# Optimization experiments

Hardware: AMD Instinct MI355X
Metric: run time of the kernel (lower is better)

The kernel has to match this reference:

```python
import jax, jax.numpy as jnp
import numpy as np

N_NODES = 50000
N_EDGES = 1600000


def gcn_conv(x, edge_index, W, b):
    """PyG GCNConv: linear transform, add self-loops, symmetric deg^-1/2 norm, scatter-add."""
    n = x.shape[0]
    h = x @ W  # [N, out]
    loop = jnp.arange(n)
    src = jnp.concatenate([edge_index[0], loop])
    dst = jnp.concatenate([edge_index[1], loop])
    ones = jnp.ones(src.shape[0], dtype=h.dtype)
    deg = jax.ops.segment_sum(ones, dst, num_segments=n)  # in-degree incl. self-loop
    dinv = jnp.where(deg > 0, jax.lax.rsqrt(deg), 0.0)
    norm = dinv[src] * dinv[dst]  # [E+N]
    msg = h[src] * norm[:, None]  # gathered, normalized messages
    out = jax.ops.segment_sum(msg, dst, num_segments=n)
    return out + b


def setup_inputs() -> dict:
    key = jax.random.key(0)
    k1, k2, k3, k4 = jax.random.split(key, 4)
    x = jax.random.normal(k1, (N_NODES, 512), dtype=jnp.float32)
    edge_index = jax.random.randint(k2, (2, N_EDGES), 0, N_NODES, dtype=jnp.int64)
    W1 = jax.random.normal(k3, (512, 128), dtype=jnp.float32) * (1.0 / np.sqrt(512))
    b1 = jnp.zeros((128,), dtype=jnp.float32)
    W2 = jax.random.normal(k4, (128, 40), dtype=jnp.float32) * (1.0 / np.sqrt(128))
    b2 = jnp.zeros((40,), dtype=jnp.float32)
    return {"x": x, "edge_index": edge_index, "W1": W1, "b1": b1, "W2": W2, "b2": b2}


def reference(x, edge_index, W1, b1, W2, b2):
    h = gcn_conv(x, edge_index, W1, b1)
    h = jax.nn.relu(h)
    h = gcn_conv(h, edge_index, W2, b2)
    return jax.nn.log_softmax(h, axis=1)
```

## Files before the change

### kernel.cpp

```cpp
#include <hip/hip_runtime.h>
#include <hip/hip_bf16.h>
#include <math.h>


#define FEAT1 512
#define FEAT2 128
#define FEAT3 40

typedef __attribute__((ext_vector_type(8))) short bf16x8;
typedef __attribute__((ext_vector_type(4))) float f32x4;

__device__ __forceinline__ unsigned short f2bf(float f) {
    union { float f; unsigned u; } c; c.f = f;
    unsigned r = c.u + 0x7fff + ((c.u >> 16) & 1);
    return (unsigned short)(r >> 16);
}
__device__ __forceinline__ float bf2f(unsigned v16) {
    union { unsigned u; float f; } c; c.u = v16 << 16;
    return c.f;
}

__device__ __forceinline__ bf16x8 pack_bf8(f32x4 a, f32x4 b) {
    union { __hip_bfloat162 h[4]; bf16x8 v; } u;
    u.h[0] = __float22bfloat162_rn(make_float2(a[0], a[1]));
    u.h[1] = __float22bfloat162_rn(make_float2(a[2], a[3]));
    u.h[2] = __float22bfloat162_rn(make_float2(b[0], b[1]));
    u.h[3] = __float22bfloat162_rn(make_float2(b[2], b[3]));
    return u.v;
}

__device__ __forceinline__ int load_src(const int* ei, long e, long E, int f64) {
    return f64 ? ei[2 * e] : ei[e];
}
__device__ __forceinline__ int load_dst(const int* ei, long e, long E, int f64) {
    return f64 ? ei[2 * E + 2 * e] : ei[E + e];
}

__launch_bounds__(1024)
__global__ void partA_kernel(const int* __restrict__ ei,
                             int* __restrict__ gbkt, unsigned* __restrict__ part,
                             int bktCap, long E, int NB) {
    __shared__ int hist[256], lbase[256], lcur[256];
    __shared__ int anyv;
    int t = threadIdx.x;
    if (t == 0) anyv = 0;
    if (t < 256) { hist[t] = 0; lcur[t] = 0; }
    __syncthreads();
    if (t < 256 && ei[2 * t + 1] != 0) anyv = 1;
    __syncthreads();
    int f64 = (anyv == 0) ? 1 : 0;

    long chunk = (E + gridDim.x - 1) / gridDim.x;
    long start = (long)blockIdx.x * chunk;
    long end = start + chunk; if (end > E) end = E;

    for (long e0 = start; e0 < end; e0 += 1024) {
        long e = e0 + t;
        if (e < end) {
            int dst = load_dst(ei, e, E, f64);
            atomicAdd(&hist[dst >> 8], 1);
        }
    }
    __syncthreads();
    if (t < NB && hist[t]) lbase[t] = atomicAdd(&gbkt[t], hist[t]);
    __syncthreads();

    for (long e0 = start; e0 < end; e0 += 1024) {
        long e = e0 + t;
        if (e < end) {
            int src = load_src(ei, e, E, f64);
            int dst = load_dst(ei, e, E, f64);
            int bkt = dst >> 8;
            int pos = lbase[bkt] + atomicAdd(&lcur[bkt], 1);
            if (pos < bktCap)
                part[(long)bkt * bktCap + pos] = (unsigned)src | ((unsigned)(dst & 255) << 17);
        }
    }
}

__launch_bounds__(256)
__global__ void partB_kernel(const unsigned* __restrict__ part, int bktCap,
                             const int* __restrict__ gbkt,
                             int* __restrict__ offsets, float* __restrict__ dinv,
                             int* __restrict__ col, int N, int E) {
    __shared__ int h[256], sc[256], cur[256];
    int b = blockIdx.x, t = threadIdx.x;
    int NB = gridDim.x;

    sc[t] = (t < NB) ? gbkt[t] : 0;
    __syncthreads();
    #pragma unroll
    for (int d = 1; d < 256; d <<= 1) {
        int tv = (t >= d) ? sc[t - d] : 0;
        __syncthreads();
        sc[t] += tv;
        __syncthreads();
    }
    int base = (b == 0) ? 0 : sc[b - 1];
    if (b == 0 && t == 0) offsets[N] = E;

    int n = gbkt[b]; if (n > bktCap) n = bktCap;
    int lo = b << 8;
    const unsigned* p = part + (long)b * bktCap;
    h[t] = 0;
    __syncthreads();
    for (int i = t; i < n; i += 256) atomicAdd(&h[(p[i] >> 17) & 255], 1);
    __syncthreads();
    int cnt = h[t];
    sc[t] = cnt;
    __syncthreads();
    #pragma unroll
    for (int d = 1; d < 256; d <<= 1) {
        int tv = (t >= d) ? sc[t - d] : 0;
        __syncthreads();
        sc[t] += tv;
        __syncthreads();
    }
    int ex = sc[t] - cnt;
    int node = lo + t;
    if (node < N) {
        offsets[node] = base + ex;
        dinv[node] = 1.0f / sqrtf((float)(cnt + 1));
    }
    cur[t] = ex;
    __syncthreads();
    for (int i = t; i < n; i += 256) {
        unsigned u = p[i];
        int r = atomicAdd(&cur[(u >> 17) & 255], 1);
        col[base + r] = u & 0x1FFFF;
    }
}

__global__ void wbt_kernel(const float* __restrict__ W1, const float* __restrict__ W2,
                           unsigned short* __restrict__ Bt, unsigned short* __restrict__ Bt2,
                           int* __restrict__ gbkt) {
    int b = blockIdx.x;
    if (b == 0 && threadIdx.x < 256) gbkt[threadIdx.x] = 0;
    if (b < FEAT2) {
        int r = b, x7 = r & 7;
        for (int k = threadIdx.x; k < FEAT1; k += blockDim.x) {
            int c = k >> 3, j = k & 7;
            int eo = (((c ^ x7) << 3) | j);
            Bt[(long)r * FEAT1 + eo] = f2bf(W1[(long)k * FEAT2 + r]);
        }
    } else {
        int n = b - FEAT2;
        for (int k = threadIdx.x; k < FEAT2; k += blockDim.x)
            Bt2[(long)n * FEAT2 + k] = (n < FEAT3) ? f2bf(W2[(long)k * FEAT3 + n]) : 0;
    }
}

#define G1_NW 8
__launch_bounds__(512, 2)
__global__ void gemm1_mfma_kernel(const float* __restrict__ A,
                                  const unsigned short* __restrict__ Bsw,
                                  const float* __restrict__ dinv,
                                  unsigned short* __restrict__ C, int M) {
    __shared__ unsigned short Bl[FEAT2 * FEAT1];
    int t = threadIdx.x;

    {
        uint4 tmp[16];
        #pragma unroll
        for (int r = 0; r < 16; r++)
            tmp[r] = *(const uint4*)((const char*)Bsw + (size_t)t * 16 + (size_t)r * 8192);
        #pragma unroll
        for (int r = 0; r < 16; r++)
            *(uint4*)((char*)Bl + (size_t)t * 16 + (size_t)r * 8192) = tmp[r];
    }
    __syncthreads();

    int w = t >> 6, lane = t & 63;
    int quad = lane >> 4, r15 = lane & 15;
    int row0 = (blockIdx.x * (G1_NW * 2) + w * 2) * 16;
    int x7 = r15 & 7;

    int ar0 = row0 + r15;      if (ar0 >= M) ar0 = M - 1;
    int ar1 = row0 + 16 + r15; if (ar1 >= M) ar1 = M - 1;
    const float* ap0 = A + (long)ar0 * FEAT1 + quad * 8;
    const float* ap1 = A + (long)ar1 * FEAT1 + quad * 8;

    f32x4 ra0[3][2], ra1[3][2];
    #pragma unroll
    for (int p = 0; p < 3; p++) {
        ra0[p][0] = *(const f32x4*)(ap0 + p * 32);
        ra0[p][1] = *(const f32x4*)(ap0 + p * 32 + 4);
        ra1[p][0] = *(const f32x4*)(ap1 + p * 32);
        ra1[p][1] = *(const f32x4*)(ap1 + p * 32 + 4);
    }

    f32x4 acc0[8], acc1[8];
    #pragma unroll
    for (int nt = 0; nt < 8; nt++) {
        acc0[nt] = (f32x4){0.f, 0.f, 0.f, 0.f};
        acc1[nt] = (f32x4){0.f, 0.f, 0.f, 0.f};
    }

    #pragma unroll
    for (int ks = 0; ks < 16; ks++) {
        int sl = ks % 3;
        bf16x8 af0 = pack_bf8(ra0[sl][0], ra0[sl][1]);
        bf16x8 af1 = pack_bf8(ra1[sl][0], ra1[sl][1]);
        if (ks < 13) {
            ra0[sl][0] = *(const f32x4*)(ap0 + (ks + 3) * 32);
            ra0[sl][1] = *(const f32x4*)(ap0 + (ks + 3) * 32 + 4);
            ra1[sl][0] = *(const f32x4*)(ap1 + (ks + 3) * 32);
            ra1[sl][1] = *(const f32x4*)(ap1 + (ks + 3) * 32 + 4);
        }
        #pragma unroll
        for (int nt = 0; nt < 8; nt++) {
            int eo = (nt * 16 + r15) * FEAT1 + (((ks * 4 + quad) ^ x7) << 3);
            bf16x8 bfrag = *(const bf16x8*)(Bl + eo);
            acc0[nt] = __builtin_amdgcn_mfma_f32_16x16x32_bf16(af0, bfrag, acc0[nt], 0, 0, 0);
            acc1[nt] = __builtin_amdgcn_mfma_f32_16x16x32_bf16(af1, bfrag, acc1[nt], 0, 0, 0);
        }
    }

    #pragma unroll
    for (int tile = 0; tile < 2; tile++) {
        #pragma unroll
        for (int reg = 0; reg < 4; reg++) {
            int orow = row0 + tile * 16 + quad * 4 + reg;
            if (orow < M) {
                float di = dinv[orow];
                #pragma unroll
                for (int nt = 0; nt < 8; nt++) {
                    float v = (tile == 0) ? acc0[nt][reg] : acc1[nt][reg];
                    C[(long)orow * FEAT2 + nt * 16 + r15] = f2bf(v * di);
                }
            }
        }
    }
}

__launch_bounds__(256)
__global__ void agg1_kernel(const unsigned short* __restrict__ h1s,
                            const int* __restrict__ col, const int* __restrict__ off,
                            const float* __restrict__ dinv, const float* __restrict__ b1,
                            unsigned short* __restrict__ a1, int N) {
    int node = blockIdx.x * 4 + (threadIdx.x >> 6);
    if (node >= N) return;
    int l = threadIdx.x & 63;
    int q = l >> 4, j = l & 15;
    const unsigned short* hp = h1s + 8 * j;
    int o0 = off[node], o1 = off[node + 1];
    float s0 = 0.f, s1 = 0.f, s2 = 0.f, s3 = 0.f,
          s4 = 0.f, s5 = 0.f, s6 = 0.f, s7 = 0.f;

    #define ACC8(P)                                                     \
        do {                                                            \
            s0 += __uint_as_float((P).x << 16);                         \
            s1 += __uint_as_float((P).x & 0xffff0000u);                 \
            s2 += __uint_as_float((P).y << 16);                         \
            s3 += __uint_as_float((P).y & 0xffff0000u);                 \
            s4 += __uint_as_float((P).z << 16);                         \
            s5 += __uint_as_float((P).z & 0xffff0000u);                 \
            s6 += __uint_as_float((P).w << 16);                         \
            s7 += __uint_as_float((P).w & 0xffff0000u);                 \
        } while (0)

    for (int base = o0; base < o1; base += 64) {
        int cnt = min(64, o1 - base);
        int myc = (l < cnt) ? col[base + l] : 0;
        int quads = cnt >> 2;
        int i = 0;
        for (; i + 2 <= quads; i += 2) {
            int c0 = __shfl(myc, 4 * i + q);
            int c1 = __shfl(myc, 4 * i + 4 + q);
            uint4 p0 = *(const uint4*)(hp + (long)c0 * FEAT2);
            uint4 p1 = *(const uint4*)(hp + (long)c1 * FEAT2);
            ACC8(p0);
            ACC8(p1);
        }
        if (i < quads) {
            int c0 = __shfl(myc, 4 * i + q);
            uint4 p0 = *(const uint4*)(hp + (long)c0 * FEAT2);
            ACC8(p0);
        }
        int e = (quads << 2) + q;
        int ec = e < 64 ? e : 0;
        int ct = __shfl(myc, ec);
        if (e < cnt) {
            uint4 p0 = *(const uint4*)(hp + (long)ct * FEAT2);
            ACC8(p0);
        }
    }
    #undef ACC8

    s0 += __shfl_xor(s0, 16); s1 += __shfl_xor(s1, 16);
    s2 += __shfl_xor(s2, 16); s3 += __shfl_xor(s3, 16);
    s4 += __shfl_xor(s4, 16); s5 += __shfl_xor(s5, 16);
    s6 += __shfl_xor(s6, 16); s7 += __shfl_xor(s7, 16);
    s0 += __shfl_xor(s0, 32); s1 += __shfl_xor(s1, 32);
    s2 += __shfl_xor(s2, 32); s3 += __shfl_xor(s3, 32);
    s4 += __shfl_xor(s4, 32); s5 += __shfl_xor(s5, 32);
    s6 += __shfl_xor(s6, 32); s7 += __shfl_xor(s7, 32);

    if (q == 0) {
        uint4 pv = *(const uint4*)(hp + (long)node * FEAT2);
        s0 += __uint_as_float(pv.x << 16); s1 += __uint_as_float(pv.x & 0xffff0000u);
        s2 += __uint_as_float(pv.y << 16); s3 += __uint_as_float(pv.y & 0xffff0000u);
        s4 += __uint_as_float(pv.z << 16); s5 += __uint_as_float(pv.z & 0xffff0000u);
        s6 += __uint_as_float(pv.w << 16); s7 += __uint_as_float(pv.w & 0xffff0000u);
        float di = dinv[node];
        float4 ba = *(const float4*)(b1 + 8 * j);
        float4 bb = *(const float4*)(b1 + 8 * j + 4);
        float v0 = s0 * di + ba.x, v1 = s1 * di + ba.y;
        float v2 = s2 * di + ba.z, v3 = s3 * di + ba.w;
        float v4 = s4 * di + bb.x, v5 = s5 * di + bb.y;
        float v6 = s6 * di + bb.z, v7 = s7 * di + bb.w;
        v0 = v0 > 0.f ? v0 : 0.f; v1 = v1 > 0.f ? v1 : 0.f;
        v2 = v2 > 0.f ? v2 : 0.f; v3 = v3 > 0.f ? v3 : 0.f;
        v4 = v4 > 0.f ? v4 : 0.f; v5 = v5 > 0.f ? v5 : 0.f;
        v6 = v6 > 0.f ? v6 : 0.f; v7 = v7 > 0.f ? v7 : 0.f;
        uint4 o;
        o.x = (unsigned)f2bf(v0) | ((unsigned)f2bf(v1) << 16);
        o.y = (unsigned)f2bf(v2) | ((unsigned)f2bf(v3) << 16);
        o.z = (unsigned)f2bf(v4) | ((unsigned)f2bf(v5) << 16);
        o.w = (unsigned)f2bf(v6) | ((unsigned)f2bf(v7) << 16);
        *(uint4*)(a1 + (long)node * FEAT2 + 8 * j) = o;
    }
}

__launch_bounds__(256)
__global__ void gemm2_mfma_kernel(const unsigned short* __restrict__ A,
                                  const unsigned short* __restrict__ Bt2,
                                  const float* __restrict__ dinv,
                                  unsigned short* __restrict__ C, int M) {
    int wave = blockIdx.x * (blockDim.x >> 6) + (threadIdx.x >> 6);
    int lane = threadIdx.x & 63;
    int quad = lane >> 4, r15 = lane & 15;
    int row0 = wave * 16;
    if (row0 >= M) return;
    int arow = row0 + r15;
    if (arow >= M) arow = M - 1;

    bf16x8 af[4];
    const unsigned short* ap = A + (long)arow * FEAT2 + quad * 8;
    #pragma unroll
    for (int ks = 0; ks < 4; ks++) af[ks] = *(const bf16x8*)(ap + ks * 32);

    f32x4 acc[3];
    #pragma unroll
    for (int nt = 0; nt < 3; nt++) acc[nt] = (f32x4){0.f, 0.f, 0.f, 0.f};
    #pragma unroll
    for (int ks = 0; ks < 4; ks++) {
        #pragma unroll
        for (int nt = 0; nt < 3; nt++) {
            bf16x8 bf = *(const bf16x8*)(Bt2 + (long)(nt * 16 + r15) * FEAT2 + ks * 32 + quad * 8);
            acc[nt] = __builtin_amdgcn_mfma_f32_16x16x32_bf16(af[ks], bf, acc[nt], 0, 0, 0);
        }
    }

    #pragma unroll
    for (int reg = 0; reg < 4; reg++) {
        int orow = row0 + quad * 4 + reg;
        if (orow >= M) continue;
        float di = dinv[orow];
        #pragma unroll
        for (int nt = 0; nt < 3; nt++) {
            int ocol = nt * 16 + r15;
            if (ocol < FEAT3)
                C[(long)orow * FEAT3 + ocol] = f2bf(acc[nt][reg] * di);
        }
    }
}

__launch_bounds__(256)
__global__ void agg2_lsm_kernel(const unsigned short* __restrict__ h2s,
                                const int* __restrict__ col, const int* __restrict__ off,
                                const float* __restrict__ dinv, const float* __restrict__ b2,
                                float* __restrict__ out, int N) {
    int node = blockIdx.x * 4 + (threadIdx.x >> 6);
    if (node >= N) return;
    int l = threadIdx.x & 63;
    bool act = l < FEAT3 / 2;
    int o0 = off[node], o1 = off[node + 1];
    float ax = 0.f, ay = 0.f;
    for (int base = o0; base < o1; base += 64) {
        int cnt = min(64, o1 - base);
        int myc = (l < cnt) ? col[base + l] : 0;
        int e = 0;
        for (; e + 4 <= cnt; e += 4) {
            int s0 = __shfl(myc, e + 0);
            int s1 = __shfl(myc, e + 1);
            int s2 = __shfl(myc, e + 2);
            int s3 = __shfl(myc, e + 3);
            if (act) {
                unsigned p0 = *(const unsigned*)(h2s + (long)s0 * FEAT3 + 2 * l);
                unsigned p1 = *(const unsigned*)(h2s + (long)s1 * FEAT3 + 2 * l);
                unsigned p2 = *(const unsigned*)(h2s + (long)s2 * FEAT3 + 2 * l);
                unsigned p3 = *(const unsigned*)(h2s + (long)s3 * FEAT3 + 2 * l);
                ax += bf2f(p0 & 0xffffu) + bf2f(p1 & 0xffffu) +
                      bf2f(p2 & 0xffffu) + bf2f(p3 & 0xffffu);
                ay += bf2f(p0 >> 16) + bf2f(p1 >> 16) + bf2f(p2 >> 16) + bf2f(p3 >> 16);
            }
        }
        for (; e < cnt; ++e) {
            int s = __shfl(myc, e);
            if (act) {
                unsigned p = *(const unsigned*)(h2s + (long)s * FEAT3 + 2 * l);
                ax += bf2f(p & 0xffffu);
                ay += bf2f(p >> 16);
            }
        }
    }
    float vx = -INFINITY, vy = -INFINITY;
    if (act) {
        unsigned pv = *(const unsigned*)(h2s + (long)node * FEAT3 + 2 * l);
        float di = dinv[node];
        float2 b = *(const float2*)(b2 + 2 * l);
        vx = (ax + bf2f(pv & 0xffffu)) * di + b.x;
        vy = (ay + bf2f(pv >> 16)) * di + b.y;
    }
    float m = fmaxf(vx, vy);
    #pragma unroll
    for (int o = 32; o >= 1; o >>= 1) m = fmaxf(m, __shfl_xor(m, o));
    float e = act ? (expf(vx - m) + expf(vy - m)) : 0.f;
    #pragma unroll
    for (int o = 32; o >= 1; o >>= 1) e += __shfl_xor(e, o);
    float ls = logf(e);
    if (act) {
        *(float2*)(out + (long)node * FEAT3 + 2 * l) = make_float2(vx - m - ls, vy - m - ls);
    }
}

extern "C" void kernel_launch(void* const* d_in, const int* in_sizes, int n_in,
                              void* d_out, int out_size, void* d_ws, size_t ws_size,
                              hipStream_t stream) {
    const float* x  = (const float*)d_in[0];
    const int*   ei = (const int*)d_in[1];
    const float* W1 = (const float*)d_in[2];
    const float* b1 = (const float*)d_in[3];
    const float* W2 = (const float*)d_in[4];
    const float* b2 = (const float*)d_in[5];
    float* out = (float*)d_out;

    const int  N = in_sizes[0] / FEAT1;
    const long E = in_sizes[1] / 2;

    char* ws = (char*)d_ws;
    size_t off = 0;
    auto alloc = [&](size_t bytes) -> void* {
        off = (off + 255) & ~(size_t)255;
        void* p = ws + off;
        off += bytes;
        return p;
    };
    const int NB = (N + 255) >> 8;
    const int bktCap = (int)(E / NB) + 1024;
    int*   offsets = (int*)alloc((size_t)(N + 1) * 4);
    float* dinv    = (float*)alloc((size_t)N * 4);
    int*   col     = (int*)alloc((size_t)E * 4);
    unsigned short* h1s = (unsigned short*)alloc((size_t)N * FEAT2 * 2);
    unsigned short* a1  = (unsigned short*)alloc((size_t)N * FEAT2 * 2);
    unsigned short* h2s = (unsigned short*)alloc((size_t)N * FEAT3 * 2);
    unsigned short* Bt  = (unsigned short*)alloc((size_t)FEAT2 * FEAT1 * 2);
    unsigned short* Bt2 = (unsigned short*)alloc((size_t)48 * FEAT2 * 2);
    unsigned* part = (unsigned*)alloc((size_t)NB * bktCap * 4);
    int*   gbkt    = (int*)alloc(256 * 4);
    int*   flagp   = (int*)alloc(4);
    (void)flagp;

    wbt_kernel<<<176, 256, 0, stream>>>(W1, W2, Bt, Bt2, gbkt);
    partA_kernel<<<256, 1024, 0, stream>>>(ei, gbkt, part, bktCap, E, NB);
    partB_kernel<<<NB, 256, 0, stream>>>(part, bktCap, gbkt, offsets, dinv, col, N, (int)E);
    {
        int tiles  = (N + 15) / 16;
        int blocks = (tiles + G1_NW * 2 - 1) / (G1_NW * 2);
        gemm1_mfma_kernel<<<blocks, 512, 0, stream>>>(x, Bt, dinv, h1s, N);
    }
    agg1_kernel<<<(N + 3) / 4, 256, 0, stream>>>(h1s, col, offsets, dinv, b1, a1, N);
    gemm2_mfma_kernel<<<(N / 16 + 3) / 4, 256, 0, stream>>>(a1, Bt2, dinv, h2s, N);
    agg2_lsm_kernel<<<(N + 3) / 4, 256, 0, stream>>>(h2s, col, offsets, dinv, b2, out, N);
}
```

Baseline: 318.7 us.

## Split agg1 into two feature-half passes, widen agg2 gathers, register-cache edges in partition

The layer-1 aggregation now runs as two launches, each covering 64 of the 128 features, so eight edges are gathered concurrently per wavefront and each pass touches a smaller slice of h1s. The layer-2 aggregation with log-softmax now uses 16-lane groups, each loading four bf16 features per edge, so four edges are processed in parallel and the partial sums are reduced with shuffles. The partition kernel keeps each thread's seven edges in registers between the histogram pass and the scatter pass instead of reading the edge list twice. The tradeoffs are a second pass over the CSR column data and two extra reduction stages, and EPT=7 only covers every edge when each block's chunk is at most 7×1024 edges, which holds for the grid size used here.

```diff
diff --git a/kernel.cpp b/kernel.cpp
--- a/kernel.cpp
+++ b/kernel.cpp
@@ -29,13 +29,7 @@
     return u.v;
 }
 
-__device__ __forceinline__ int load_src(const int* ei, long e, long E, int f64) {
-    return f64 ? ei[2 * e] : ei[e];
-}
-__device__ __forceinline__ int load_dst(const int* ei, long e, long E, int f64) {
-    return f64 ? ei[2 * E + 2 * e] : ei[E + e];
-}
-
+#define EPT 7
 __launch_bounds__(1024)
 __global__ void partA_kernel(const int* __restrict__ ei,
                              int* __restrict__ gbkt, unsigned* __restrict__ part,
@@ -49,31 +43,40 @@
     if (t < 256 && ei[2 * t + 1] != 0) anyv = 1;
     __syncthreads();
     int f64 = (anyv == 0) ? 1 : 0;
+    const long long* ei64 = (const long long*)ei;
 
     long chunk = (E + gridDim.x - 1) / gridDim.x;
     long start = (long)blockIdx.x * chunk;
     long end = start + chunk; if (end > E) end = E;
 
-    for (long e0 = start; e0 < end; e0 += 1024) {
-        long e = e0 + t;
+    int srcs[EPT], dsts[EPT];
+    #pragma unroll
+    for (int r = 0; r < EPT; r++) {
+        long e = start + (long)r * 1024 + t;
         if (e < end) {
-            int dst = load_dst(ei, e, E, f64);
-            atomicAdd(&hist[dst >> 8], 1);
+            if (f64) {
+                srcs[r] = (int)ei64[e];
+                dsts[r] = (int)ei64[E + e];
+            } else {
+                srcs[r] = ei[e];
+                dsts[r] = ei[E + e];
+            }
+            atomicAdd(&hist[dsts[r] >> 8], 1);
         }
     }
     __syncthreads();
     if (t < NB && hist[t]) lbase[t] = atomicAdd(&gbkt[t], hist[t]);
     __syncthreads();
 
-    for (long e0 = start; e0 < end; e0 += 1024) {
-        long e = e0 + t;
+    #pragma unroll
+    for (int r = 0; r < EPT; r++) {
+        long e = start + (long)r * 1024 + t;
         if (e < end) {
-            int src = load_src(ei, e, E, f64);
-            int dst = load_dst(ei, e, E, f64);
-            int bkt = dst >> 8;
+            int bkt = dsts[r] >> 8;
             int pos = lbase[bkt] + atomicAdd(&lcur[bkt], 1);
             if (pos < bktCap)
-                part[(long)bkt * bktCap + pos] = (unsigned)src | ((unsigned)(dst & 255) << 17);
+                part[(long)bkt * bktCap + pos] =
+                    (unsigned)srcs[r] | ((unsigned)(dsts[r] & 255) << 17);
         }
     }
 }
@@ -237,12 +240,12 @@
 __global__ void agg1_kernel(const unsigned short* __restrict__ h1s,
                             const int* __restrict__ col, const int* __restrict__ off,
                             const float* __restrict__ dinv, const float* __restrict__ b1,
-                            unsigned short* __restrict__ a1, int N) {
+                            unsigned short* __restrict__ a1, int N, int fofs) {
     int node = blockIdx.x * 4 + (threadIdx.x >> 6);
     if (node >= N) return;
     int l = threadIdx.x & 63;
-    int q = l >> 4, j = l & 15;
-    const unsigned short* hp = h1s + 8 * j;
+    int q = l >> 3, j = l & 7;
+    const unsigned short* hp = h1s + fofs + 8 * j;
     int o0 = off[node], o1 = off[node + 1];
     float s0 = 0.f, s1 = 0.f, s2 = 0.f, s3 = 0.f,
           s4 = 0.f, s5 = 0.f, s6 = 0.f, s7 = 0.f;
@@ -262,24 +265,23 @@
     for (int base = o0; base < o1; base += 64) {
         int cnt = min(64, o1 - base);
         int myc = (l < cnt) ? col[base + l] : 0;
-        int quads = cnt >> 2;
+        int octs = cnt >> 3;
         int i = 0;
-        for (; i + 2 <= quads; i += 2) {
-            int c0 = __shfl(myc, 4 * i + q);
-            int c1 = __shfl(myc, 4 * i + 4 + q);
+        for (; i + 2 <= octs; i += 2) {
+            int c0 = __shfl(myc, 8 * i + q);
+            int c1 = __shfl(myc, 8 * i + 8 + q);
             uint4 p0 = *(const uint4*)(hp + (long)c0 * FEAT2);
             uint4 p1 = *(const uint4*)(hp + (long)c1 * FEAT2);
             ACC8(p0);
             ACC8(p1);
         }
-        if (i < quads) {
-            int c0 = __shfl(myc, 4 * i + q);
+        if (i < octs) {
+            int c0 = __shfl(myc, 8 * i + q);
             uint4 p0 = *(const uint4*)(hp + (long)c0 * FEAT2);
             ACC8(p0);
         }
-        int e = (quads << 2) + q;
-        int ec = e < 64 ? e : 0;
-        int ct = __shfl(myc, ec);
+        int e = (octs << 3) + q;
+        int ct = __shfl(myc, e);
         if (e < cnt) {
             uint4 p0 = *(const uint4*)(hp + (long)ct * FEAT2);
             ACC8(p0);
@@ -287,6 +289,10 @@
     }
     #undef ACC8
 
+    s0 += __shfl_xor(s0, 8);  s1 += __shfl_xor(s1, 8);
+    s2 += __shfl_xor(s2, 8);  s3 += __shfl_xor(s3, 8);
+    s4 += __shfl_xor(s4, 8);  s5 += __shfl_xor(s5, 8);
+    s6 += __shfl_xor(s6, 8);  s7 += __shfl_xor(s7, 8);
     s0 += __shfl_xor(s0, 16); s1 += __shfl_xor(s1, 16);
     s2 += __shfl_xor(s2, 16); s3 += __shfl_xor(s3, 16);
     s4 += __shfl_xor(s4, 16); s5 += __shfl_xor(s5, 16);
@@ -296,15 +302,15 @@
     s4 += __shfl_xor(s4, 32); s5 += __shfl_xor(s5, 32);
     s6 += __shfl_xor(s6, 32); s7 += __shfl_xor(s7, 32);
 
-    if (q == 0) {
+    if (l < 8) {
         uint4 pv = *(const uint4*)(hp + (long)node * FEAT2);
         s0 += __uint_as_float(pv.x << 16); s1 += __uint_as_float(pv.x & 0xffff0000u);
         s2 += __uint_as_float(pv.y << 16); s3 += __uint_as_float(pv.y & 0xffff0000u);
         s4 += __uint_as_float(pv.z << 16); s5 += __uint_as_float(pv.z & 0xffff0000u);
         s6 += __uint_as_float(pv.w << 16); s7 += __uint_as_float(pv.w & 0xffff0000u);
         float di = dinv[node];
-        float4 ba = *(const float4*)(b1 + 8 * j);
-        float4 bb = *(const float4*)(b1 + 8 * j + 4);
+        float4 ba = *(const float4*)(b1 + fofs + 8 * j);
+        float4 bb = *(const float4*)(b1 + fofs + 8 * j + 4);
         float v0 = s0 * di + ba.x, v1 = s1 * di + ba.y;
         float v2 = s2 * di + ba.z, v3 = s3 * di + ba.w;
         float v4 = s4 * di + bb.x, v5 = s5 * di + bb.y;
@@ -318,7 +324,7 @@
         o.y = (unsigned)f2bf(v2) | ((unsigned)f2bf(v3) << 16);
         o.z = (unsigned)f2bf(v4) | ((unsigned)f2bf(v5) << 16);
         o.w = (unsigned)f2bf(v6) | ((unsigned)f2bf(v7) << 16);
-        *(uint4*)(a1 + (long)node * FEAT2 + 8 * j) = o;
+        *(uint4*)(a1 + (long)node * FEAT2 + fofs + 8 * j) = o;
     }
 }
 
@@ -374,54 +380,76 @@
     int node = blockIdx.x * 4 + (threadIdx.x >> 6);
     if (node >= N) return;
     int l = threadIdx.x & 63;
-    bool act = l < FEAT3 / 2;
+    int q = l >> 4, jj = l & 15;
+    bool act = jj < 10;
+    const unsigned short* hp = h2s + 4 * jj;
     int o0 = off[node], o1 = off[node + 1];
-    float ax = 0.f, ay = 0.f;
+    float s0 = 0.f, s1 = 0.f, s2 = 0.f, s3 = 0.f;
+
+    #define ACC4(P)                                                     \
+        do {                                                            \
+            s0 += __uint_as_float((P).x << 16);                         \
+            s1 += __uint_as_float((P).x & 0xffff0000u);                 \
+            s2 += __uint_as_float((P).y << 16);                         \
+            s3 += __uint_as_float((P).y & 0xffff0000u);                 \
+        } while (0)
+
     for (int base = o0; base < o1; base += 64) {
         int cnt = min(64, o1 - base);
         int myc = (l < cnt) ? col[base + l] : 0;
-        int e = 0;
-        for (; e + 4 <= cnt; e += 4) {
-            int s0 = __shfl(myc, e + 0);
-            int s1 = __shfl(myc, e + 1);
-            int s2 = __shfl(myc, e + 2);
-            int s3 = __shfl(myc, e + 3);
+        int quads = cnt >> 2;
+        int i = 0;
+        for (; i + 2 <= quads; i += 2) {
+            int c0 = __shfl(myc, 4 * i + q);
+            int c1 = __shfl(myc, 4 * i + 4 + q);
             if (act) {
-                unsigned p0 = *(const unsigned*)(h2s + (long)s0 * FEAT3 + 2 * l);
-                unsigned p1 = *(const unsigned*)(h2s + (long)s1 * FEAT3 + 2 * l);
-                unsigned p2 = *(const unsigned*)(h2s + (long)s2 * FEAT3 + 2 * l);
-                unsigned p3 = *(const unsigned*)(h2s + (long)s3 * FEAT3 + 2 * l);
-                ax += bf2f(p0 & 0xffffu) + bf2f(p1 & 0xffffu) +
-                      bf2f(p2 & 0xffffu) + bf2f(p3 & 0xffffu);
-                ay += bf2f(p0 >> 16) + bf2f(p1 >> 16) + bf2f(p2 >> 16) + bf2f(p3 >> 16);
+                uint2 p0 = *(const uint2*)(hp + (long)c0 * FEAT3);
+                uint2 p1 = *(const uint2*)(hp + (long)c1 * FEAT3);
+                ACC4(p0);
+                ACC4(p1);
             }
         }
-        for (; e < cnt; ++e) {
-            int s = __shfl(myc, e);
+        if (i < quads) {
+            int c0 = __shfl(myc, 4 * i + q);
             if (act) {
-                unsigned p = *(const unsigned*)(h2s + (long)s * FEAT3 + 2 * l);
-                ax += bf2f(p & 0xffffu);
-                ay += bf2f(p >> 16);
+                uint2 p0 = *(const uint2*)(hp + (long)c0 * FEAT3);
+                ACC4(p0);
             }
         }
-    }
-    float vx = -INFINITY, vy = -INFINITY;
+        int e = (quads << 2) + q;
+        int ct = __shfl(myc, e);
+        if (e < cnt && act) {
+            uint2 p0 = *(const uint2*)(hp + (long)ct * FEAT3);
+            ACC4(p0);
+        }
+    }
+    #undef ACC4
+
+    s0 += __shfl_xor(s0, 16); s1 += __shfl_xor(s1, 16);
+    s2 += __shfl_xor(s2, 16); s3 += __shfl_xor(s3, 16);
+    s0 += __shfl_xor(s0, 32); s1 += __shfl_xor(s1, 32);
+    s2 += __shfl_xor(s2, 32); s3 += __shfl_xor(s3, 32);
+
+    float v0 = -INFINITY, v1 = -INFINITY, v2 = -INFINITY, v3 = -INFINITY;
     if (act) {
-        unsigned pv = *(const unsigned*)(h2s + (long)node * FEAT3 + 2 * l);
+        uint2 pv = *(const uint2*)(hp + (long)node * FEAT3);
+        s0 += __uint_as_float(pv.x << 16); s1 += __uint_as_float(pv.x & 0xffff0000u);
+        s2 += __uint_as_float(pv.y << 16); s3 += __uint_as_float(pv.y & 0xffff0000u);
         float di = dinv[node];
-        float2 b = *(const float2*)(b2 + 2 * l);
-        vx = (ax + bf2f(pv & 0xffffu)) * di + b.x;
-        vy = (ay + bf2f(pv >> 16)) * di + b.y;
-    }
-    float m = fmaxf(vx, vy);
-    #pragma unroll
-    for (int o = 32; o >= 1; o >>= 1) m = fmaxf(m, __shfl_xor(m, o));
-    float e = act ? (expf(vx - m) + expf(vy - m)) : 0.f;
-    #pragma unroll
-    for (int o = 32; o >= 1; o >>= 1) e += __shfl_xor(e, o);
+        float4 b = *(const float4*)(b2 + 4 * jj);
+        v0 = s0 * di + b.x; v1 = s1 * di + b.y;
+        v2 = s2 * di + b.z; v3 = s3 * di + b.w;
+    }
+    float m = fmaxf(fmaxf(v0, v1), fmaxf(v2, v3));
+    #pragma unroll
+    for (int o = 1; o < 16; o <<= 1) m = fmaxf(m, __shfl_xor(m, o));
+    float e = act ? (expf(v0 - m) + expf(v1 - m) + expf(v2 - m) + expf(v3 - m)) : 0.f;
+    #pragma unroll
+    for (int o = 1; o < 16; o <<= 1) e += __shfl_xor(e, o);
     float ls = logf(e);
-    if (act) {
-        *(float2*)(out + (long)node * FEAT3 + 2 * l) = make_float2(vx - m - ls, vy - m - ls);
+    if (q == 0 && act) {
+        *(float4*)(out + (long)node * FEAT3 + 4 * jj) =
+            make_float4(v0 - m - ls, v1 - m - ls, v2 - m - ls, v3 - m - ls);
     }
 }
 
@@ -459,8 +487,6 @@
     unsigned short* Bt2 = (unsigned short*)alloc((size_t)48 * FEAT2 * 2);
     unsigned* part = (unsigned*)alloc((size_t)NB * bktCap * 4);
     int*   gbkt    = (int*)alloc(256 * 4);
-    int*   flagp   = (int*)alloc(4);
-    (void)flagp;
 
     wbt_kernel<<<176, 256, 0, stream>>>(W1, W2, Bt, Bt2, gbkt);
     partA_kernel<<<256, 1024, 0, stream>>>(ei, gbkt, part, bktCap, E, NB);
@@ -470,7 +496,8 @@
         int blocks = (tiles + G1_NW * 2 - 1) / (G1_NW * 2);
         gemm1_mfma_kernel<<<blocks, 512, 0, stream>>>(x, Bt, dinv, h1s, N);
     }
-    agg1_kernel<<<(N + 3) / 4, 256, 0, stream>>>(h1s, col, offsets, dinv, b1, a1, N);
+    agg1_kernel<<<(N + 3) / 4, 256, 0, stream>>>(h1s, col, offsets, dinv, b1, a1, N, 0);
+    agg1_kernel<<<(N + 3) / 4, 256, 0, stream>>>(h1s, col, offsets, dinv, b1, a1, N, 64);
     gemm2_mfma_kernel<<<(N / 16 + 3) / 4, 256, 0, stream>>>(a1, Bt2, dinv, h2s, N);
     agg2_lsm_kernel<<<(N + 3) / 4, 256, 0, stream>>>(h2s, col, offsets, dinv, b2, out, N);
 }
```

Result: no change. 312.7 us (-1.9%).
